# Kernel optimization log

Hardware: AMD Instinct MI355X
Metric: run time of the kernel (lower is better)

The kernel has to match this reference:

```python
import jax, jax.numpy as jnp
import numpy as np

BLADES = ["", "1", "2", "12"]   # quaternion blades (upstride_type=2)
GEOM = (0, 2, 0)                  # e1^2 = e2^2 = -1


def _square_vector(idx):
    if idx < GEOM[0] + 1:
        return 1
    if idx < GEOM[0] + GEOM[1] + 1:
        return -1
    return 0


def _ga_mul(index_1, index_2):
    # faithful port of GenericLinear._ga_multiply_get_index (compile-time, pure python)
    l1 = [int(c) for c in index_1]
    l2 = [int(c) for c in index_2]
    s, i1, i2, length_l1 = 1, 0, 0, len(l1)
    out_l = []
    while i1 < len(l1) and i2 < len(l2):
        if l1[i1] == l2[i2]:
            if (length_l1 - 1) % 2 != 0:
                s *= -1
            s *= _square_vector(l1[i1])
            length_l1 -= 1
            i1 += 1
            i2 += 1
        elif l1[i1] > l2[i2]:
            if length_l1 % 2 != 0:
                s *= -1
            out_l.append(l2[i2])
            i2 += 1
        else:
            out_l.append(l1[i1])
            length_l1 -= 1
            i1 += 1
    out_l += l1[i1:] + l2[i2:]
    return s, "".join(str(v) for v in out_l)


def _cayley():
    N = len(BLADES)
    tbl = []
    for i in range(N):
        row = []
        for j in range(N):
            s, idx = _ga_mul(BLADES[i], BLADES[j])
            row.append((BLADES.index(idx), s))
        tbl.append(row)
    return tbl


def setup_inputs() -> dict:
    key = jax.random.key(0)
    k1, k2, k3 = jax.random.split(key, 3)
    N, BS, Cin, U = 4, 16384, 256, 256
    x = jax.random.normal(k1, (N * BS, Cin), dtype=jnp.float32)
    W = jax.random.normal(k2, (Cin, N * U), dtype=jnp.float32) * 0.02
    b = jax.random.normal(k3, (N * U,), dtype=jnp.float32) * 0.01
    return {"x": x, "W": W, "b": b}


def reference(x, W, b):
    N = len(BLADES)
    BS = x.shape[0] // N
    U = W.shape[1] // N
    y = x @ W                      # (N*BS, N*U) -- the wrapped Dense (use_bias stripped)
    y = y.reshape(N, BS, N * U)
    y = y.at[0].add(b)             # BiasLayer applied to blade-0 batch chunk only
    cross = y.reshape(N, BS, N, U) # cross[i, :, j, :] = x-blade-i through weight-blade-j
    tbl = _cayley()
    out = [None] * N
    for i in range(N):
        for j in range(N):
            k, s = tbl[i][j]
            t = cross[i, :, j, :] if s == 1 else -cross[i, :, j, :]
            out[k] = t if out[k] is None else out[k] + t
    return jnp.concatenate(out, axis=0)   # (N*BS, U)
```

## Files before the change

### kernel.cpp

```cpp
#include <hip/hip_runtime.h>

using u32 = unsigned int;

typedef __attribute__((ext_vector_type(8))) _Float16 f16x8;
typedef __attribute__((ext_vector_type(4))) float    f32x4;

__global__ __launch_bounds__(256) void build_wcatT(const float* __restrict__ W,
                                                   _Float16* __restrict__ Wt) {
    int t  = blockIdx.x * 256 + threadIdx.x;
    int n  = t >> 10, kk = t & 1023;
    int kb = n >> 8,  u  = n & 255;
    int i  = kk >> 8, c  = kk & 255;
    int j  = i ^ kb;
    float v = W[c * 1024 + j * 256 + u];
    if ((0x3950u >> (i * 4 + kb)) & 1u) v = -v;
    Wt[t] = (_Float16)v;
}

__device__ __forceinline__ void async16(const void* g, void* l) {
    __builtin_amdgcn_global_load_lds((const __attribute__((address_space(1))) u32*)g,
                                     (__attribute__((address_space(3))) u32*)l,
                                     16, 0, 0);
}

#define BARRIER() do { asm volatile("" ::: "memory"); \
                       __builtin_amdgcn_s_barrier(); \
                       asm volatile("" ::: "memory"); } while (0)

#define VMW(n)  asm volatile("s_waitcnt vmcnt(" #n ")" ::: "memory")
#define LGKM0() asm volatile("s_waitcnt lgkmcnt(0)" ::: "memory")
#define SB0()   __builtin_amdgcn_sched_barrier(0)

#define GL16(dst, ptr, off) \
    asm volatile("global_load_dwordx4 %0, %1, off offset:" #off \
                 : "=v"(dst) : "v"(ptr))

#define MFMA(av, bv, c) __builtin_amdgcn_mfma_f32_16x16x32_f16(av, bv, c, 0, 0, 0)

#define PHASE16() do { \
    __builtin_amdgcn_s_setprio(1); \
    acc[0][0]=MFMA(af0,bf0,acc[0][0]); acc[0][1]=MFMA(af0,bf1,acc[0][1]); \
    acc[0][2]=MFMA(af0,bf2,acc[0][2]); acc[0][3]=MFMA(af0,bf3,acc[0][3]); \
    acc[1][0]=MFMA(af1,bf0,acc[1][0]); acc[1][1]=MFMA(af1,bf1,acc[1][1]); \
    acc[1][2]=MFMA(af1,bf2,acc[1][2]); acc[1][3]=MFMA(af1,bf3,acc[1][3]); \
    acc[2][0]=MFMA(af2,bf0,acc[2][0]); acc[2][1]=MFMA(af2,bf1,acc[2][1]); \
    acc[2][2]=MFMA(af2,bf2,acc[2][2]); acc[2][3]=MFMA(af2,bf3,acc[2][3]); \
    acc[3][0]=MFMA(af3,bf0,acc[3][0]); acc[3][1]=MFMA(af3,bf1,acc[3][1]); \
    acc[3][2]=MFMA(af3,bf2,acc[3][2]); acc[3][3]=MFMA(af3,bf3,acc[3][3]); \
    __builtin_amdgcn_s_setprio(0); \
    __builtin_amdgcn_sched_barrier(0); \
} while (0)

#define ISSUE_A(U, d0, d1, d2, d3) do { \
    const float* _p = pA + (size_t)((U) >> 3) * 4194304 + ((U) & 7) * 32; \
    GL16(d0, _p, 0); GL16(d1, _p, 16); GL16(d2, _p, 32); GL16(d3, _p, 48); \
} while (0)

#define STAGE_B(U, SB) do { \
    async16(gB0 + (U) * 32, lds + (SB) * 8192 + 4096 + tid * 8); \
    async16(gB1 + (U) * 32, lds + (SB) * 8192 + 6144 + tid * 8); \
} while (0)

#define WRITE_A(WBUF, s0, s1, s2, s3) do { \
    f16x8 h0, h1; \
    h0[0]=(_Float16)(s0)[0]; h0[1]=(_Float16)(s0)[1]; \
    h0[2]=(_Float16)(s0)[2]; h0[3]=(_Float16)(s0)[3]; \
    h0[4]=(_Float16)(s1)[0]; h0[5]=(_Float16)(s1)[1]; \
    h0[6]=(_Float16)(s1)[2]; h0[7]=(_Float16)(s1)[3]; \
    h1[0]=(_Float16)(s2)[0]; h1[1]=(_Float16)(s2)[1]; \
    h1[2]=(_Float16)(s2)[2]; h1[3]=(_Float16)(s2)[3]; \
    h1[4]=(_Float16)(s3)[0]; h1[5]=(_Float16)(s3)[1]; \
    h1[6]=(_Float16)(s3)[2]; h1[7]=(_Float16)(s3)[3]; \
    _Float16* _wp = lds + (WBUF) * 8192; \
    *(f16x8*)(_wp + awoff0) = h0; \
    *(f16x8*)(_wp + awoff1) = h1; \
} while (0)

#define TILE(T, BUF, SBUF, WBUF, DO_ISSUE, I0,I1,I2,I3, DO_WRITE, W0,W1,W2,W3, GATE) do { \
    const _Float16* Ab = lds + (BUF) * 8192; \
    f16x8 af0, af1, af2, af3, bf0, bf1, bf2, bf3; \
    af0 = *(const f16x8*)(Ab + aoff);        af1 = *(const f16x8*)(Ab + aoff + 512); \
    af2 = *(const f16x8*)(Ab + aoff + 1024); af3 = *(const f16x8*)(Ab + aoff + 1536); \
    bf0 = *(const f16x8*)(Ab + boff);        bf1 = *(const f16x8*)(Ab + boff + 512); \
    bf2 = *(const f16x8*)(Ab + boff + 1024); bf3 = *(const f16x8*)(Ab + boff + 1536); \
    if (DO_ISSUE) { ISSUE_A((T) + 2, I0, I1, I2, I3); STAGE_B((T) + 2, SBUF); } \
    PHASE16(); \
    GATE; \
    SB0(); \
    if (DO_WRITE) { WRITE_A(WBUF, W0, W1, W2, W3); } \
    LGKM0(); \
    BARRIER(); \
} while (0)

__global__ __launch_bounds__(256, 2) void ga_gemm(const float* __restrict__ A,
                                                  const _Float16* __restrict__ Bt,
                                                  const float*  __restrict__ bias,
                                                  float* __restrict__ out) {
    __shared__ _Float16 lds[3 * 8192] __attribute__((aligned(16)));

    const int tid  = threadIdx.x;
    const int lane = tid & 63;
    const int wid  = tid >> 6;
    const int wm   = wid >> 1;
    const int wn   = wid & 1;
    const int l15  = lane & 15;
    const int lg   = lane >> 4;

    const int bid = blockIdx.x;
    const int xcd = bid & 7, idx = bid >> 3;
    const int nt  = idx & 7;
    const int mt  = (idx >> 3) * 8 + xcd;
    const int m0  = mt * 128, n0 = nt * 128;

    const int ar = tid >> 1, ah = tid & 1;
    const float* pA = A + (size_t)(m0 + ar) * 256 + ah * 16;
    const int aph = (ar >> 1) & 3;
    const int awoff0 = ar * 32 + ((ah * 2)     ^ aph) * 8;
    const int awoff1 = ar * 32 + ((ah * 2 + 1) ^ aph) * 8;

    const int br = tid >> 2;
    const int bg = (tid & 3) ^ ((br >> 1) & 3);
    const _Float16* gB0 = Bt + (size_t)(n0 + br) * 1024 + bg * 8;
    const _Float16* gB1 = gB0 + 64 * 1024;

    const int sc   = lg ^ ((l15 >> 1) & 3);
    const int aoff = (wm * 64 + l15) * 32 + sc * 8;
    const int boff = 4096 + (wn * 64 + l15) * 32 + sc * 8;

    f32x4 acc[4][4] = {};
    f32x4 u0, u1, u2, u3, v0, v1, v2, v3;

    ISSUE_A(0, u0, u1, u2, u3);  STAGE_B(0, 0);
    ISSUE_A(1, v0, v1, v2, v3);  STAGE_B(1, 1);
    VMW(6);  SB0();
    WRITE_A(0, u0, u1, u2, u3);
    LGKM0();
    BARRIER();

    for (int t = 0; t < 30; t += 6) {
        TILE(t + 0, 0, 2, 1, 1, u0,u1,u2,u3, 1, v0,v1,v2,v3, VMW(6));
        TILE(t + 1, 1, 0, 2, 1, v0,v1,v2,v3, 1, u0,u1,u2,u3, VMW(6));
        TILE(t + 2, 2, 1, 0, 1, u0,u1,u2,u3, 1, v0,v1,v2,v3, VMW(6));
        TILE(t + 3, 0, 2, 1, 1, v0,v1,v2,v3, 1, u0,u1,u2,u3, VMW(6));
        TILE(t + 4, 1, 0, 2, 1, u0,u1,u2,u3, 1, v0,v1,v2,v3, VMW(6));
        TILE(t + 5, 2, 1, 0, 1, v0,v1,v2,v3, 1, u0,u1,u2,u3, VMW(6));
    }
    TILE(30, 0, 0, 1, 0, u0,u1,u2,u3, 1, v0,v1,v2,v3, VMW(0));
    TILE(31, 1, 0, 0, 0, u0,u1,u2,u3, 0, u0,u1,u2,u3, (void)0);

    const int kb   = nt >> 1;
    const int ucol = (nt & 1) * 128 + wn * 64 + l15;
    float bv[4];
#pragma unroll
    for (int fn = 0; fn < 4; ++fn) bv[fn] = bias[nt * 128 + wn * 64 + fn * 16 + l15];
#pragma unroll
    for (int fm = 0; fm < 4; ++fm) {
        const int m = m0 + wm * 64 + fm * 16 + lg * 4;
#pragma unroll
        for (int r = 0; r < 4; ++r) {
            float* op = out + ((size_t)kb * 16384 + m + r) * 256 + ucol;
#pragma unroll
            for (int fn = 0; fn < 4; ++fn)
                op[fn * 16] = acc[fm][fn][r] + bv[fn];
        }
    }
}

extern "C" void kernel_launch(void* const* d_in, const int* in_sizes, int n_in,
                              void* d_out, int out_size, void* d_ws, size_t ws_size,
                              hipStream_t stream) {
    (void)in_sizes; (void)n_in; (void)out_size; (void)ws_size;
    const float* x = (const float*)d_in[0];
    const float* W = (const float*)d_in[1];
    const float* b = (const float*)d_in[2];
    float* out = (float*)d_out;

    _Float16* Wt = (_Float16*)d_ws;

    build_wcatT<<<4096, 256, 0, stream>>>(W, Wt);
    ga_gemm<<<1024, 256, 0, stream>>>(x, Wt, b, out);
}
```

Measured before the change: 63.89 us.

## Stage fp32 A tiles directly into LDS and widen blocks to 256x128

The GEMM now copies fp32 activation tiles straight into LDS with asynchronous global-to-LDS loads and converts them to fp16 when reading fragments, instead of loading into registers, converting, and writing to LDS. Blocks grow to 512 threads covering 256 rows, with a K-step of 64, a double-buffered LDS scheme with XOR swizzles, and a new block-to-tile mapping. This aims to cut register pressure and VALU/LDS-write overhead and to halve B reloads. In exchange it doubles the LDS footprint to 160 KB per block. It also waits for all outstanding loads every iteration, which may expose memory latency.

```diff
diff --git a/kernel.cpp b/kernel.cpp
--- a/kernel.cpp
+++ b/kernel.cpp
@@ -28,75 +28,76 @@
                        asm volatile("" ::: "memory"); } while (0)
 
 #define VMW(n)  asm volatile("s_waitcnt vmcnt(" #n ")" ::: "memory")
-#define LGKM0() asm volatile("s_waitcnt lgkmcnt(0)" ::: "memory")
-#define SB0()   __builtin_amdgcn_sched_barrier(0)
-
-#define GL16(dst, ptr, off) \
-    asm volatile("global_load_dwordx4 %0, %1, off offset:" #off \
-                 : "=v"(dst) : "v"(ptr))
 
 #define MFMA(av, bv, c) __builtin_amdgcn_mfma_f32_16x16x32_f16(av, bv, c, 0, 0, 0)
 
-#define PHASE16() do { \
+#define MM16() do { \
     __builtin_amdgcn_s_setprio(1); \
-    acc[0][0]=MFMA(af0,bf0,acc[0][0]); acc[0][1]=MFMA(af0,bf1,acc[0][1]); \
-    acc[0][2]=MFMA(af0,bf2,acc[0][2]); acc[0][3]=MFMA(af0,bf3,acc[0][3]); \
-    acc[1][0]=MFMA(af1,bf0,acc[1][0]); acc[1][1]=MFMA(af1,bf1,acc[1][1]); \
-    acc[1][2]=MFMA(af1,bf2,acc[1][2]); acc[1][3]=MFMA(af1,bf3,acc[1][3]); \
-    acc[2][0]=MFMA(af2,bf0,acc[2][0]); acc[2][1]=MFMA(af2,bf1,acc[2][1]); \
-    acc[2][2]=MFMA(af2,bf2,acc[2][2]); acc[2][3]=MFMA(af2,bf3,acc[2][3]); \
-    acc[3][0]=MFMA(af3,bf0,acc[3][0]); acc[3][1]=MFMA(af3,bf1,acc[3][1]); \
-    acc[3][2]=MFMA(af3,bf2,acc[3][2]); acc[3][3]=MFMA(af3,bf3,acc[3][3]); \
+    acc[0][0]=MFMA(a0,b0,acc[0][0]); acc[0][1]=MFMA(a0,b1,acc[0][1]); \
+    acc[0][2]=MFMA(a0,b2,acc[0][2]); acc[0][3]=MFMA(a0,b3,acc[0][3]); \
+    acc[1][0]=MFMA(a1,b0,acc[1][0]); acc[1][1]=MFMA(a1,b1,acc[1][1]); \
+    acc[1][2]=MFMA(a1,b2,acc[1][2]); acc[1][3]=MFMA(a1,b3,acc[1][3]); \
+    acc[2][0]=MFMA(a2,b0,acc[2][0]); acc[2][1]=MFMA(a2,b1,acc[2][1]); \
+    acc[2][2]=MFMA(a2,b2,acc[2][2]); acc[2][3]=MFMA(a2,b3,acc[2][3]); \
+    acc[3][0]=MFMA(a3,b0,acc[3][0]); acc[3][1]=MFMA(a3,b1,acc[3][1]); \
+    acc[3][2]=MFMA(a3,b2,acc[3][2]); acc[3][3]=MFMA(a3,b3,acc[3][3]); \
     __builtin_amdgcn_s_setprio(0); \
     __builtin_amdgcn_sched_barrier(0); \
 } while (0)
 
-#define ISSUE_A(U, d0, d1, d2, d3) do { \
-    const float* _p = pA + (size_t)((U) >> 3) * 4194304 + ((U) & 7) * 32; \
-    GL16(d0, _p, 0); GL16(d1, _p, 16); GL16(d2, _p, 32); GL16(d3, _p, 48); \
+#define ISSUE_A(U, BO) do { \
+    const float* _b = pA + (size_t)((U) >> 2) * 4194304 + ((U) & 3) * 64; \
+    float* _d = ldsf + (BO) + tid * 4; \
+    async16(_b,         _d);         async16(_b +  8192, _d + 2048); \
+    async16(_b + 16384, _d + 4096);  async16(_b + 24576, _d + 6144); \
+    async16(_b + 32768, _d + 8192);  async16(_b + 40960, _d + 10240); \
+    async16(_b + 49152, _d + 12288); async16(_b + 57344, _d + 14336); \
 } while (0)
 
-#define STAGE_B(U, SB) do { \
-    async16(gB0 + (U) * 32, lds + (SB) * 8192 + 4096 + tid * 8); \
-    async16(gB1 + (U) * 32, lds + (SB) * 8192 + 6144 + tid * 8); \
+#define STAGE_B(U, BO) do { \
+    const _Float16* _s = gB + (U) * 64; \
+    _Float16* _d = (_Float16*)(ldsf + (BO) + 16384) + tid * 8; \
+    async16(_s, _d);  async16(_s + 65536, _d + 4096); \
 } while (0)
 
-#define WRITE_A(WBUF, s0, s1, s2, s3) do { \
-    f16x8 h0, h1; \
-    h0[0]=(_Float16)(s0)[0]; h0[1]=(_Float16)(s0)[1]; \
-    h0[2]=(_Float16)(s0)[2]; h0[3]=(_Float16)(s0)[3]; \
-    h0[4]=(_Float16)(s1)[0]; h0[5]=(_Float16)(s1)[1]; \
-    h0[6]=(_Float16)(s1)[2]; h0[7]=(_Float16)(s1)[3]; \
-    h1[0]=(_Float16)(s2)[0]; h1[1]=(_Float16)(s2)[1]; \
-    h1[2]=(_Float16)(s2)[2]; h1[3]=(_Float16)(s2)[3]; \
-    h1[4]=(_Float16)(s3)[0]; h1[5]=(_Float16)(s3)[1]; \
-    h1[6]=(_Float16)(s3)[2]; h1[7]=(_Float16)(s3)[3]; \
-    _Float16* _wp = lds + (WBUF) * 8192; \
-    *(f16x8*)(_wp + awoff0) = h0; \
-    *(f16x8*)(_wp + awoff1) = h1; \
+#define LDA(dst, Ab, F, C0, C1) do { \
+    f32x4 _q0 = *(const f32x4*)((Ab) + aRowBase + (F) * 1024 + (C0)); \
+    f32x4 _q1 = *(const f32x4*)((Ab) + aRowBase + (F) * 1024 + (C1)); \
+    dst[0]=(_Float16)_q0[0]; dst[1]=(_Float16)_q0[1]; \
+    dst[2]=(_Float16)_q0[2]; dst[3]=(_Float16)_q0[3]; \
+    dst[4]=(_Float16)_q1[0]; dst[5]=(_Float16)_q1[1]; \
+    dst[6]=(_Float16)_q1[2]; dst[7]=(_Float16)_q1[3]; \
 } while (0)
 
-#define TILE(T, BUF, SBUF, WBUF, DO_ISSUE, I0,I1,I2,I3, DO_WRITE, W0,W1,W2,W3, GATE) do { \
-    const _Float16* Ab = lds + (BUF) * 8192; \
-    f16x8 af0, af1, af2, af3, bf0, bf1, bf2, bf3; \
-    af0 = *(const f16x8*)(Ab + aoff);        af1 = *(const f16x8*)(Ab + aoff + 512); \
-    af2 = *(const f16x8*)(Ab + aoff + 1024); af3 = *(const f16x8*)(Ab + aoff + 1536); \
-    bf0 = *(const f16x8*)(Ab + boff);        bf1 = *(const f16x8*)(Ab + boff + 512); \
-    bf2 = *(const f16x8*)(Ab + boff + 1024); bf3 = *(const f16x8*)(Ab + boff + 1536); \
-    if (DO_ISSUE) { ISSUE_A((T) + 2, I0, I1, I2, I3); STAGE_B((T) + 2, SBUF); } \
-    PHASE16(); \
+#define TILE(T, DO_STAGE, GATE) do { \
+    const int _bo = ((T) & 1) * 20480; \
+    if (DO_STAGE) { ISSUE_A((T) + 1, _bo ^ 20480); STAGE_B((T) + 1, _bo ^ 20480); } \
+    const float* Ab = ldsf + _bo; \
+    const _Float16* Bb = (const _Float16*)(Ab + 16384); \
+    f16x8 a0, a1, a2, a3, b0, b1, b2, b3; \
+    LDA(a0, Ab, 0, ac00, ac01); LDA(a1, Ab, 1, ac00, ac01); \
+    LDA(a2, Ab, 2, ac00, ac01); LDA(a3, Ab, 3, ac00, ac01); \
+    b0 = *(const f16x8*)(Bb + bRowBase + bc0); \
+    b1 = *(const f16x8*)(Bb + bRowBase + 1024 + bc0); \
+    b2 = *(const f16x8*)(Bb + bRowBase + 2048 + bc0); \
+    b3 = *(const f16x8*)(Bb + bRowBase + 3072 + bc0); \
+    MM16(); \
+    LDA(a0, Ab, 0, ac10, ac11); LDA(a1, Ab, 1, ac10, ac11); \
+    LDA(a2, Ab, 2, ac10, ac11); LDA(a3, Ab, 3, ac10, ac11); \
+    b0 = *(const f16x8*)(Bb + bRowBase + bc1); \
+    b1 = *(const f16x8*)(Bb + bRowBase + 1024 + bc1); \
+    b2 = *(const f16x8*)(Bb + bRowBase + 2048 + bc1); \
+    b3 = *(const f16x8*)(Bb + bRowBase + 3072 + bc1); \
+    MM16(); \
     GATE; \
-    SB0(); \
-    if (DO_WRITE) { WRITE_A(WBUF, W0, W1, W2, W3); } \
-    LGKM0(); \
     BARRIER(); \
 } while (0)
 
-__global__ __launch_bounds__(256, 2) void ga_gemm(const float* __restrict__ A,
+__global__ __launch_bounds__(512, 2) void ga_gemm(const float* __restrict__ A,
                                                   const _Float16* __restrict__ Bt,
                                                   const float*  __restrict__ bias,
                                                   float* __restrict__ out) {
-    __shared__ _Float16 lds[3 * 8192] __attribute__((aligned(16)));
+    __shared__ float ldsf[2 * 20480] __attribute__((aligned(16)));
 
     const int tid  = threadIdx.x;
     const int lane = tid & 63;
@@ -107,61 +108,55 @@
     const int lg   = lane >> 4;
 
     const int bid = blockIdx.x;
-    const int xcd = bid & 7, idx = bid >> 3;
-    const int nt  = idx & 7;
-    const int mt  = (idx >> 3) * 8 + xcd;
-    const int m0  = mt * 128, n0 = nt * 128;
+    const int xcd = bid & 7, i2 = bid >> 3;
+    const int nt  = i2 & 7;
+    const int mt  = xcd * 8 + (i2 >> 3);
+    const int m0  = mt * 256, n0 = nt * 128;
 
-    const int ar = tid >> 1, ah = tid & 1;
-    const float* pA = A + (size_t)(m0 + ar) * 256 + ah * 16;
-    const int aph = (ar >> 1) & 3;
-    const int awoff0 = ar * 32 + ((ah * 2)     ^ aph) * 8;
-    const int awoff1 = ar * 32 + ((ah * 2 + 1) ^ aph) * 8;
+    const int sArow   = tid >> 4;
+    const int sAchunk = (tid & 15) ^ ((tid >> 4) & 15);
+    const float* pA = A + (size_t)(m0 + sArow) * 256 + sAchunk * 4;
 
-    const int br = tid >> 2;
-    const int bg = (tid & 3) ^ ((br >> 1) & 3);
-    const _Float16* gB0 = Bt + (size_t)(n0 + br) * 1024 + bg * 8;
-    const _Float16* gB1 = gB0 + 64 * 1024;
+    const int sBrow   = tid >> 3;
+    const int sBchunk = (tid & 7) ^ ((tid >> 3) & 7);
+    const _Float16* gB = Bt + (size_t)(n0 + sBrow) * 1024 + sBchunk * 8;
 
-    const int sc   = lg ^ ((l15 >> 1) & 3);
-    const int aoff = (wm * 64 + l15) * 32 + sc * 8;
-    const int boff = 4096 + (wn * 64 + l15) * 32 + sc * 8;
+    const int aRowBase = (wm * 64 + l15) * 64;
+    const int ac00 = ((lg * 2)     ^ l15) * 4;
+    const int ac01 = ((lg * 2 + 1) ^ l15) * 4;
+    const int ac10 = ((8 + lg * 2)     ^ l15) * 4;
+    const int ac11 = ((8 + lg * 2 + 1) ^ l15) * 4;
+
+    const int bRowBase = (wn * 64 + l15) * 64;
+    const int bc0 = ((lg)     ^ (l15 & 7)) * 8;
+    const int bc1 = ((4 + lg) ^ (l15 & 7)) * 8;
 
     f32x4 acc[4][4] = {};
-    f32x4 u0, u1, u2, u3, v0, v1, v2, v3;
 
-    ISSUE_A(0, u0, u1, u2, u3);  STAGE_B(0, 0);
-    ISSUE_A(1, v0, v1, v2, v3);  STAGE_B(1, 1);
-    VMW(6);  SB0();
-    WRITE_A(0, u0, u1, u2, u3);
-    LGKM0();
+    ISSUE_A(0, 0);  STAGE_B(0, 0);
+    VMW(0);
     BARRIER();
 
-    for (int t = 0; t < 30; t += 6) {
-        TILE(t + 0, 0, 2, 1, 1, u0,u1,u2,u3, 1, v0,v1,v2,v3, VMW(6));
-        TILE(t + 1, 1, 0, 2, 1, v0,v1,v2,v3, 1, u0,u1,u2,u3, VMW(6));
-        TILE(t + 2, 2, 1, 0, 1, u0,u1,u2,u3, 1, v0,v1,v2,v3, VMW(6));
-        TILE(t + 3, 0, 2, 1, 1, v0,v1,v2,v3, 1, u0,u1,u2,u3, VMW(6));
-        TILE(t + 4, 1, 0, 2, 1, u0,u1,u2,u3, 1, v0,v1,v2,v3, VMW(6));
-        TILE(t + 5, 2, 1, 0, 1, v0,v1,v2,v3, 1, u0,u1,u2,u3, VMW(6));
+    for (int t = 0; t < 15; ++t) {
+        TILE(t, 1, VMW(0));
     }
-    TILE(30, 0, 0, 1, 0, u0,u1,u2,u3, 1, v0,v1,v2,v3, VMW(0));
-    TILE(31, 1, 0, 0, 0, u0,u1,u2,u3, 0, u0,u1,u2,u3, (void)0);
+    TILE(15, 0, (void)0);
 
     const int kb   = nt >> 1;
     const int ucol = (nt & 1) * 128 + wn * 64 + l15;
     float bv[4];
 #pragma unroll
-    for (int fn = 0; fn < 4; ++fn) bv[fn] = bias[nt * 128 + wn * 64 + fn * 16 + l15];
+    for (int fn = 0; fn < 4; ++fn)
+        bv[fn] = bias[nt * 128 + wn * 64 + fn * 16 + l15];
 #pragma unroll
     for (int fm = 0; fm < 4; ++fm) {
         const int m = m0 + wm * 64 + fm * 16 + lg * 4;
 #pragma unroll
-        for (int r = 0; r < 4; ++r) {
-            float* op = out + ((size_t)kb * 16384 + m + r) * 256 + ucol;
+        for (int rr = 0; rr < 4; ++rr) {
+            float* op = out + ((size_t)kb * 16384 + m + rr) * 256 + ucol;
 #pragma unroll
             for (int fn = 0; fn < 4; ++fn)
-                op[fn * 16] = acc[fm][fn][r] + bv[fn];
+                op[fn * 16] = acc[fm][fn][rr] + bv[fn];
         }
     }
 }
@@ -178,5 +173,5 @@
     _Float16* Wt = (_Float16*)d_ws;
 
     build_wcatT<<<4096, 256, 0, stream>>>(W, Wt);
-    ga_gemm<<<1024, 256, 0, stream>>>(x, Wt, b, out);
+    ga_gemm<<<512, 512, 0, stream>>>(x, Wt, b, out);
 }
```

Result: slower. 66.21 us (+3.6%).

## Load A fragments straight to registers, skip LDS staging, use 512-thread 256-row tiles

Applied to the files above, without the earlier changes.

Each wave now loads its own fp32 A rows directly from global memory into registers in MFMA fragment layout and converts them to fp16 in-register. This removes the A write into LDS and its LDS reads. Only B is staged through a triple-buffered LDS ring, with K=64 per tile. Blocks grow to 512 threads covering 256 M rows each, and the grid is halved with a new XCD swizzle. The trade-off is that A is no longer shared through LDS across the two N-waves, so each A element is fetched twice from global/L2, and the change raises register pressure.

```diff
diff --git a/kernel.cpp b/kernel.cpp
--- a/kernel.cpp
+++ b/kernel.cpp
@@ -28,16 +28,15 @@
                        asm volatile("" ::: "memory"); } while (0)
 
 #define VMW(n)  asm volatile("s_waitcnt vmcnt(" #n ")" ::: "memory")
-#define LGKM0() asm volatile("s_waitcnt lgkmcnt(0)" ::: "memory")
 #define SB0()   __builtin_amdgcn_sched_barrier(0)
 
-#define GL16(dst, ptr, off) \
-    asm volatile("global_load_dwordx4 %0, %1, off offset:" #off \
-                 : "=v"(dst) : "v"(ptr))
+#define GLS(dst, voff, sb, OFF) \
+    asm volatile("global_load_dwordx4 %0, %1, %2 offset:" #OFF \
+                 : "=v"(dst) : "v"(voff), "s"(sb))
 
 #define MFMA(av, bv, c) __builtin_amdgcn_mfma_f32_16x16x32_f16(av, bv, c, 0, 0, 0)
 
-#define PHASE16() do { \
+#define MM16() do { \
     __builtin_amdgcn_s_setprio(1); \
     acc[0][0]=MFMA(af0,bf0,acc[0][0]); acc[0][1]=MFMA(af0,bf1,acc[0][1]); \
     acc[0][2]=MFMA(af0,bf2,acc[0][2]); acc[0][3]=MFMA(af0,bf3,acc[0][3]); \
@@ -51,52 +50,71 @@
     __builtin_amdgcn_sched_barrier(0); \
 } while (0)
 
-#define ISSUE_A(U, d0, d1, d2, d3) do { \
-    const float* _p = pA + (size_t)((U) >> 3) * 4194304 + ((U) & 7) * 32; \
-    GL16(d0, _p, 0); GL16(d1, _p, 16); GL16(d2, _p, 32); GL16(d3, _p, 48); \
-} while (0)
-
-#define STAGE_B(U, SB) do { \
-    async16(gB0 + (U) * 32, lds + (SB) * 8192 + 4096 + tid * 8); \
-    async16(gB1 + (U) * 32, lds + (SB) * 8192 + 6144 + tid * 8); \
-} while (0)
-
-#define WRITE_A(WBUF, s0, s1, s2, s3) do { \
-    f16x8 h0, h1; \
-    h0[0]=(_Float16)(s0)[0]; h0[1]=(_Float16)(s0)[1]; \
-    h0[2]=(_Float16)(s0)[2]; h0[3]=(_Float16)(s0)[3]; \
-    h0[4]=(_Float16)(s1)[0]; h0[5]=(_Float16)(s1)[1]; \
-    h0[6]=(_Float16)(s1)[2]; h0[7]=(_Float16)(s1)[3]; \
-    h1[0]=(_Float16)(s2)[0]; h1[1]=(_Float16)(s2)[1]; \
-    h1[2]=(_Float16)(s2)[2]; h1[3]=(_Float16)(s2)[3]; \
-    h1[4]=(_Float16)(s3)[0]; h1[5]=(_Float16)(s3)[1]; \
-    h1[6]=(_Float16)(s3)[2]; h1[7]=(_Float16)(s3)[3]; \
-    _Float16* _wp = lds + (WBUF) * 8192; \
-    *(f16x8*)(_wp + awoff0) = h0; \
-    *(f16x8*)(_wp + awoff1) = h1; \
-} while (0)
-
-#define TILE(T, BUF, SBUF, WBUF, DO_ISSUE, I0,I1,I2,I3, DO_WRITE, W0,W1,W2,W3, GATE) do { \
-    const _Float16* Ab = lds + (BUF) * 8192; \
-    f16x8 af0, af1, af2, af3, bf0, bf1, bf2, bf3; \
-    af0 = *(const f16x8*)(Ab + aoff);        af1 = *(const f16x8*)(Ab + aoff + 512); \
-    af2 = *(const f16x8*)(Ab + aoff + 1024); af3 = *(const f16x8*)(Ab + aoff + 1536); \
-    bf0 = *(const f16x8*)(Ab + boff);        bf1 = *(const f16x8*)(Ab + boff + 512); \
-    bf2 = *(const f16x8*)(Ab + boff + 1024); bf3 = *(const f16x8*)(Ab + boff + 1536); \
-    if (DO_ISSUE) { ISSUE_A((T) + 2, I0, I1, I2, I3); STAGE_B((T) + 2, SBUF); } \
-    PHASE16(); \
-    GATE; \
+#define ISSUE_K0(U, R) do { \
+    const float* _sb = A + (size_t)m0 * 256 + (size_t)((U) >> 2) * 4194304 + ((U) & 3) * 64; \
+    GLS(R##0, voff0, _sb, 0);  GLS(R##1, voff0, _sb, 16); \
+    GLS(R##2, voff1, _sb, 0);  GLS(R##3, voff1, _sb, 16); \
+    GLS(R##4, voff2, _sb, 0);  GLS(R##5, voff2, _sb, 16); \
+    GLS(R##6, voff3, _sb, 0);  GLS(R##7, voff3, _sb, 16); \
+} while (0)
+
+#define ISSUE_K1(U, R) do { \
+    const float* _sb = A + (size_t)m0 * 256 + (size_t)((U) >> 2) * 4194304 + ((U) & 3) * 64; \
+    GLS(R##0, voff0, _sb, 128); GLS(R##1, voff0, _sb, 144); \
+    GLS(R##2, voff1, _sb, 128); GLS(R##3, voff1, _sb, 144); \
+    GLS(R##4, voff2, _sb, 128); GLS(R##5, voff2, _sb, 144); \
+    GLS(R##6, voff3, _sb, 128); GLS(R##7, voff3, _sb, 144); \
+} while (0)
+
+#define CVTSET(R) do { \
+    af0[0]=(_Float16)R##0[0]; af0[1]=(_Float16)R##0[1]; af0[2]=(_Float16)R##0[2]; af0[3]=(_Float16)R##0[3]; \
+    af0[4]=(_Float16)R##1[0]; af0[5]=(_Float16)R##1[1]; af0[6]=(_Float16)R##1[2]; af0[7]=(_Float16)R##1[3]; \
+    af1[0]=(_Float16)R##2[0]; af1[1]=(_Float16)R##2[1]; af1[2]=(_Float16)R##2[2]; af1[3]=(_Float16)R##2[3]; \
+    af1[4]=(_Float16)R##3[0]; af1[5]=(_Float16)R##3[1]; af1[6]=(_Float16)R##3[2]; af1[7]=(_Float16)R##3[3]; \
+    af2[0]=(_Float16)R##4[0]; af2[1]=(_Float16)R##4[1]; af2[2]=(_Float16)R##4[2]; af2[3]=(_Float16)R##4[3]; \
+    af2[4]=(_Float16)R##5[0]; af2[5]=(_Float16)R##5[1]; af2[6]=(_Float16)R##5[2]; af2[7]=(_Float16)R##5[3]; \
+    af3[0]=(_Float16)R##6[0]; af3[1]=(_Float16)R##6[1]; af3[2]=(_Float16)R##6[2]; af3[3]=(_Float16)R##6[3]; \
+    af3[4]=(_Float16)R##7[0]; af3[5]=(_Float16)R##7[1]; af3[6]=(_Float16)R##7[2]; af3[7]=(_Float16)R##7[3]; \
+} while (0)
+
+#define STAGE_B(U, BI) do { \
+    const _Float16* _s = gB + (U) * 64; \
+    _Float16* _d = ldsB + (BI) * 8192 + tid * 8; \
+    async16(_s, _d); \
+    async16(_s + 65536, _d + 4096); \
+} while (0)
+
+#define TILE(T, BI, G1, G2, DO_NEXT, DO_STAGE, G3, DO_BAR) do { \
+    const _Float16* Bb = ldsB + (BI) * 8192; \
+    f16x8 af0, af1, af2, af3; \
+    G1; SB0(); \
+    CVTSET(p); \
+    if (DO_NEXT) { ISSUE_K0((T) + 1, p); } \
     SB0(); \
-    if (DO_WRITE) { WRITE_A(WBUF, W0, W1, W2, W3); } \
-    LGKM0(); \
-    BARRIER(); \
-} while (0)
-
-__global__ __launch_bounds__(256, 2) void ga_gemm(const float* __restrict__ A,
+    { f16x8 bf0 = *(const f16x8*)(Bb + bRow + bc0); \
+      f16x8 bf1 = *(const f16x8*)(Bb + bRow + 1024 + bc0); \
+      f16x8 bf2 = *(const f16x8*)(Bb + bRow + 2048 + bc0); \
+      f16x8 bf3 = *(const f16x8*)(Bb + bRow + 3072 + bc0); \
+      MM16(); } \
+    G2; SB0(); \
+    CVTSET(q); \
+    if (DO_NEXT) { ISSUE_K1((T) + 1, q); } \
+    SB0(); \
+    { f16x8 bf0 = *(const f16x8*)(Bb + bRow + bc1); \
+      f16x8 bf1 = *(const f16x8*)(Bb + bRow + 1024 + bc1); \
+      f16x8 bf2 = *(const f16x8*)(Bb + bRow + 2048 + bc1); \
+      f16x8 bf3 = *(const f16x8*)(Bb + bRow + 3072 + bc1); \
+      MM16(); } \
+    if (DO_STAGE) { STAGE_B((T) + 2, ((T) + 2) % 3); } \
+    G3; \
+    if (DO_BAR) { BARRIER(); } \
+} while (0)
+
+__global__ __launch_bounds__(512, 2) void ga_gemm(const float* __restrict__ A,
                                                   const _Float16* __restrict__ Bt,
                                                   const float*  __restrict__ bias,
                                                   float* __restrict__ out) {
-    __shared__ _Float16 lds[3 * 8192] __attribute__((aligned(16)));
+    __shared__ _Float16 ldsB[3 * 8192] __attribute__((aligned(16)));
 
     const int tid  = threadIdx.x;
     const int lane = tid & 63;
@@ -107,61 +125,66 @@
     const int lg   = lane >> 4;
 
     const int bid = blockIdx.x;
-    const int xcd = bid & 7, idx = bid >> 3;
-    const int nt  = idx & 7;
-    const int mt  = (idx >> 3) * 8 + xcd;
-    const int m0  = mt * 128, n0 = nt * 128;
-
-    const int ar = tid >> 1, ah = tid & 1;
-    const float* pA = A + (size_t)(m0 + ar) * 256 + ah * 16;
-    const int aph = (ar >> 1) & 3;
-    const int awoff0 = ar * 32 + ((ah * 2)     ^ aph) * 8;
-    const int awoff1 = ar * 32 + ((ah * 2 + 1) ^ aph) * 8;
-
-    const int br = tid >> 2;
-    const int bg = (tid & 3) ^ ((br >> 1) & 3);
-    const _Float16* gB0 = Bt + (size_t)(n0 + br) * 1024 + bg * 8;
-    const _Float16* gB1 = gB0 + 64 * 1024;
-
-    const int sc   = lg ^ ((l15 >> 1) & 3);
-    const int aoff = (wm * 64 + l15) * 32 + sc * 8;
-    const int boff = 4096 + (wn * 64 + l15) * 32 + sc * 8;
+    const int swz = (bid & 7) * 64 + (bid >> 3);
+    const int mt  = swz >> 3, nt = swz & 7;
+    const int m0  = mt * 256, n0 = nt * 128;
+
+    const u32 voff0 = (u32)(((wm * 64 +  0 + l15) * 256 + lg * 8) * 4);
+    const u32 voff1 = (u32)(((wm * 64 + 16 + l15) * 256 + lg * 8) * 4);
+    const u32 voff2 = (u32)(((wm * 64 + 32 + l15) * 256 + lg * 8) * 4);
+    const u32 voff3 = (u32)(((wm * 64 + 48 + l15) * 256 + lg * 8) * 4);
+
+    const int brow = tid >> 3;
+    const int blc  = (tid & 7) ^ (brow & 7);
+    const _Float16* gB = Bt + (size_t)(n0 + brow) * 1024 + blc * 8;
+
+    const int bRow = wn * 4096 + l15 * 64;
+    const int bc0  = ((lg)     ^ (l15 & 7)) * 8;
+    const int bc1  = ((4 + lg) ^ (l15 & 7)) * 8;
 
     f32x4 acc[4][4] = {};
-    f32x4 u0, u1, u2, u3, v0, v1, v2, v3;
-
-    ISSUE_A(0, u0, u1, u2, u3);  STAGE_B(0, 0);
-    ISSUE_A(1, v0, v1, v2, v3);  STAGE_B(1, 1);
-    VMW(6);  SB0();
-    WRITE_A(0, u0, u1, u2, u3);
-    LGKM0();
+    f32x4 p0, p1, p2, p3, p4, p5, p6, p7;
+    f32x4 q0, q1, q2, q3, q4, q5, q6, q7;
+
+    ISSUE_K0(0, p);
+    ISSUE_K1(0, q);
+    STAGE_B(0, 0);
+    STAGE_B(1, 1);
+    VMW(2);
     BARRIER();
 
-    for (int t = 0; t < 30; t += 6) {
-        TILE(t + 0, 0, 2, 1, 1, u0,u1,u2,u3, 1, v0,v1,v2,v3, VMW(6));
-        TILE(t + 1, 1, 0, 2, 1, v0,v1,v2,v3, 1, u0,u1,u2,u3, VMW(6));
-        TILE(t + 2, 2, 1, 0, 1, u0,u1,u2,u3, 1, v0,v1,v2,v3, VMW(6));
-        TILE(t + 3, 0, 2, 1, 1, v0,v1,v2,v3, 1, u0,u1,u2,u3, VMW(6));
-        TILE(t + 4, 1, 0, 2, 1, u0,u1,u2,u3, 1, v0,v1,v2,v3, VMW(6));
-        TILE(t + 5, 2, 1, 0, 1, v0,v1,v2,v3, 1, u0,u1,u2,u3, VMW(6));
-    }
-    TILE(30, 0, 0, 1, 0, u0,u1,u2,u3, 1, v0,v1,v2,v3, VMW(0));
-    TILE(31, 1, 0, 0, 0, u0,u1,u2,u3, 0, u0,u1,u2,u3, (void)0);
-
-    const int kb   = nt >> 1;
-    const int ucol = (nt & 1) * 128 + wn * 64 + l15;
+    TILE( 0, 0, VMW(10), VMW(10), 1, 1, VMW(18), 1);
+    TILE( 1, 1, VMW(10), VMW(10), 1, 1, VMW(18), 1);
+    TILE( 2, 2, VMW(10), VMW(10), 1, 1, VMW(18), 1);
+    TILE( 3, 0, VMW(10), VMW(10), 1, 1, VMW(18), 1);
+    TILE( 4, 1, VMW(10), VMW(10), 1, 1, VMW(18), 1);
+    TILE( 5, 2, VMW(10), VMW(10), 1, 1, VMW(18), 1);
+    TILE( 6, 0, VMW(10), VMW(10), 1, 1, VMW(18), 1);
+    TILE( 7, 1, VMW(10), VMW(10), 1, 1, VMW(18), 1);
+    TILE( 8, 2, VMW(10), VMW(10), 1, 1, VMW(18), 1);
+    TILE( 9, 0, VMW(10), VMW(10), 1, 1, VMW(18), 1);
+    TILE(10, 1, VMW(10), VMW(10), 1, 1, VMW(18), 1);
+    TILE(11, 2, VMW(10), VMW(10), 1, 1, VMW(18), 1);
+    TILE(12, 0, VMW(10), VMW(10), 1, 1, VMW(18), 1);
+    TILE(13, 1, VMW(10), VMW(10), 1, 1, VMW(18), 1);
+    TILE(14, 2, VMW(10), VMW(10), 1, 0, VMW(16), 1);
+    TILE(15, 0, VMW(8),  VMW(0),  0, 0, (void)0, 0);
+
+    const int nbase = nt * 128 + wn * 64;
+    const int kb    = nbase >> 8;
+    const int ub    = (nbase & 255) + l15;
     float bv[4];
 #pragma unroll
-    for (int fn = 0; fn < 4; ++fn) bv[fn] = bias[nt * 128 + wn * 64 + fn * 16 + l15];
+    for (int fn = 0; fn < 4; ++fn) bv[fn] = bias[nbase + fn * 16 + l15];
 #pragma unroll
     for (int fm = 0; fm < 4; ++fm) {
         const int m = m0 + wm * 64 + fm * 16 + lg * 4;
 #pragma unroll
-        for (int r = 0; r < 4; ++r) {
-            float* op = out + ((size_t)kb * 16384 + m + r) * 256 + ucol;
+        for (int rr = 0; rr < 4; ++rr) {
+            float* op = out + ((size_t)kb * 16384 + m + rr) * 256 + ub;
 #pragma unroll
             for (int fn = 0; fn < 4; ++fn)
-                op[fn * 16] = acc[fm][fn][r] + bv[fn];
+                op[fn * 16] = acc[fm][fn][rr] + bv[fn];
         }
     }
 }
@@ -178,5 +201,5 @@
     _Float16* Wt = (_Float16*)d_ws;
 
     build_wcatT<<<4096, 256, 0, stream>>>(W, Wt);
-    ga_gemm<<<1024, 256, 0, stream>>>(x, Wt, b, out);
-}
+    ga_gemm<<<512, 512, 0, stream>>>(x, Wt, b, out);
+}
```

Result: slower. 136.8 us (+114.1%).
